# Performance work log

Hardware: AMD Instinct MI355X
Metric: run time of the kernel (lower is better)

Reference implementation:

```python
import jax, jax.numpy as jnp
import numpy as np

N = 100000
E = 1600000
DIN = 128
H = 4
C1 = 32   # hidden_dim per head, layer 1
C2 = 64   # output_dim, layer 2 (heads=1)
NEG_SLOPE = 0.2


def setup_inputs() -> dict:
    key = jax.random.key(0)
    ks = jax.random.split(key, 16)
    x = jax.random.normal(ks[0], (N, DIN), dtype=jnp.float32)
    src = jax.random.randint(ks[1], (E,), 0, N, dtype=jnp.int64)
    off = jax.random.randint(ks[2], (E,), 1, N, dtype=jnp.int64)
    dst = (src + off) % N  # guaranteed no self loops
    edge_index = jnp.stack([src, dst], axis=0)
    edge_weight = jax.random.uniform(ks[3], (E,), dtype=jnp.float32)
    g = 0.1
    # layer 1 params (heads=4, concat)
    W1 = jax.random.normal(ks[4], (DIN, H * C1), dtype=jnp.float32) * g
    att_src1 = jax.random.normal(ks[5], (H, C1), dtype=jnp.float32) * g
    att_dst1 = jax.random.normal(ks[6], (H, C1), dtype=jnp.float32) * g
    att_edge1 = jax.random.normal(ks[7], (H, C1), dtype=jnp.float32) * g
    We1 = jax.random.normal(ks[8], (1, H * C1), dtype=jnp.float32) * g
    b1 = jnp.zeros((H * C1,), dtype=jnp.float32)
    # layer 2 params (heads=1, no concat)
    W2 = jax.random.normal(ks[9], (H * C1, C2), dtype=jnp.float32) * g
    att_src2 = jax.random.normal(ks[10], (1, C2), dtype=jnp.float32) * g
    att_dst2 = jax.random.normal(ks[11], (1, C2), dtype=jnp.float32) * g
    att_edge2 = jax.random.normal(ks[12], (1, C2), dtype=jnp.float32) * g
    We2 = jax.random.normal(ks[13], (1, C2), dtype=jnp.float32) * g
    b2 = jnp.zeros((C2,), dtype=jnp.float32)
    return dict(x=x, edge_index=edge_index, edge_weight=edge_weight,
                W1=W1, att_src1=att_src1, att_dst1=att_dst1, att_edge1=att_edge1, We1=We1, b1=b1,
                W2=W2, att_src2=att_src2, att_dst2=att_dst2, att_edge2=att_edge2, We2=We2, b2=b2)


def gat_conv(x, src, dst, ew, W, a_src, a_dst, a_edge, We, b, heads, out_ch, concat):
    n = x.shape[0]
    xs = (x @ W).reshape(n, heads, out_ch)                 # [N,H,C]
    alpha_src = (xs * a_src[None]).sum(-1)                 # [N,H]
    alpha_dst = (xs * a_dst[None]).sum(-1)                 # [N,H]
    e = (ew[:, None] @ We).reshape(-1, heads, out_ch)      # [E,H,C]
    alpha_edge = (e * a_edge[None]).sum(-1)                # [E,H]
    alpha = alpha_src[src] + alpha_dst[dst] + alpha_edge   # [E,H]
    alpha = jax.nn.leaky_relu(alpha, NEG_SLOPE)
    # segment softmax over destination nodes (every node has a self loop)
    m = jax.ops.segment_max(alpha, dst, num_segments=n)
    ex = jnp.exp(alpha - m[dst])
    s = jax.ops.segment_sum(ex, dst, num_segments=n)
    att = ex / (s[dst] + 1e-16)                            # [E,H]
    out = jax.ops.segment_sum(xs[src] * att[:, :, None], dst, num_segments=n)  # [N,H,C]
    out = out.reshape(n, heads * out_ch) if concat else out.mean(axis=1)
    return out + b


def reference(x, edge_index, edge_weight,
              W1, att_src1, att_dst1, att_edge1, We1, b1,
              W2, att_src2, att_dst2, att_edge2, We2, b2):
    n = x.shape[0]
    src, dst = edge_index[0], edge_index[1]
    # add self loops with fill_value='mean' for edge weights (PyG default)
    si = jnp.arange(n, dtype=src.dtype)
    src2 = jnp.concatenate([src, si])
    dst2 = jnp.concatenate([dst, si])
    ew2 = jnp.concatenate([edge_weight, jnp.full((n,), edge_weight.mean(), dtype=edge_weight.dtype)])
    h = gat_conv(x, src2, dst2, ew2, W1, att_src1, att_dst1, att_edge1, We1, b1, H, C1, True)
    h = jax.nn.elu(h)
    # dropout is identity in eval mode
    out = gat_conv(h, src2, dst2, ew2, W2, att_src2, att_dst2, att_edge2, We2, b2, 1, C2, False)
    return out
```

## Files before the change

### kernel.cpp

```cpp
#include <hip/hip_runtime.h>
#include <math.h>

#define NN 100000
#define NE 1600000
#define DIN 128
#define NH 4
#define C1 32
#define C2 64
#define NEG 0.2f

#define SCAN_CHUNK 1024
#define NBLK ((NN + SCAN_CHUNK - 1) / SCAN_CHUNK)

#define NBUCK 8
#define BUCKN (NN / NBUCK)
#define CAPB 300000
#define BIN_CHUNK 4096
#define NBINBLK ((NE + BIN_CHUNK - 1) / BIN_CHUNK)

__device__ __forceinline__ unsigned bf16rtn(float f) {
    unsigned b = __float_as_uint(f);
    return (b + 0x7FFFu + ((b >> 16) & 1u)) >> 16;
}
__device__ __forceinline__ unsigned pack2bf(float lo, float hi) {
    return bf16rtn(lo) | (bf16rtn(hi) << 16);
}

__global__ void k_setup(const float* __restrict__ We1, const float* __restrict__ ae1,
                        const float* __restrict__ We2, const float* __restrict__ ae2,
                        float* __restrict__ params) {
    __shared__ float sm[128];
    int t = threadIdx.x;
    sm[t] = We1[t] * ae1[t];
    __syncthreads();
    if (t < 4) {
        float s = 0.f;
        for (int c = 0; c < 32; c++) s += sm[t * 32 + c];
        params[2 + t] = s;
    }
    __syncthreads();
    if (t < 64) sm[t] = We2[t] * ae2[t];
    __syncthreads();
    if (t == 0) {
        float s = 0.f;
        for (int c = 0; c < 64; c++) s += sm[c];
        params[6] = s;
        params[1] = params[0] / (float)NE;
    }
}

__global__ void k_binA(const int* __restrict__ srcI, const int* __restrict__ dstI,
                       const float* __restrict__ ew, int* __restrict__ bcur,
                       int* __restrict__ bdst, int2* __restrict__ bse,
                       float* __restrict__ params) {
    __shared__ int hcnt[NBUCK], hbase[NBUCK], hoff[NBUCK];
    int t = threadIdx.x;
    int e0 = blockIdx.x * BIN_CHUNK;
    if (t < NBUCK) hcnt[t] = 0;
    __syncthreads();
    for (int i = t; i < BIN_CHUNK; i += 256) {
        int e = e0 + i;
        if (e < NE) atomicAdd(&hcnt[dstI[e] / BUCKN], 1);
    }
    __syncthreads();
    if (t < NBUCK) { hbase[t] = atomicAdd(&bcur[t], hcnt[t]); hoff[t] = 0; }
    __syncthreads();
    float locw = 0.f;
    for (int i = t; i < BIN_CHUNK; i += 256) {
        int e = e0 + i;
        if (e < NE) {
            int d = dstI[e];
            float w = ew[e];
            locw += w;
            int b = d / BUCKN;
            int p = b * CAPB + hbase[b] + atomicAdd(&hoff[b], 1);
            bdst[p] = d;
            bse[p] = make_int2(srcI[e], __float_as_int(w));
        }
    }
    for (int o = 32; o > 0; o >>= 1) locw += __shfl_down(locw, o, 64);
    if ((t & 63) == 0) atomicAdd(&params[0], locw);
}

__global__ void k_histB(const int* __restrict__ bdst, const int* __restrict__ bcur,
                        int* __restrict__ deg) {
    int b = blockIdx.x & (NBUCK - 1);
    int slice = blockIdx.x >> 3;
    int cnt = bcur[b];
    int lo = b * CAPB;
    int per = (cnt + 255) / 256;
    int s0 = lo + slice * per;
    int s1 = min(s0 + per, lo + cnt);
    for (int i = s0 + threadIdx.x; i < s1; i += 256)
        atomicAdd(&deg[bdst[i]], 1);
}

__global__ void k_scanA(const int* __restrict__ deg, int* __restrict__ bsum) {
    __shared__ int ws[4];
    int b = blockIdx.x;
    int base = b * SCAN_CHUNK;
    int t = threadIdx.x;
    int s = 0;
    for (int i = t; i < SCAN_CHUNK; i += 256) {
        int idx = base + i;
        if (idx < NN) s += deg[idx];
    }
    for (int o = 32; o > 0; o >>= 1) s += __shfl_down(s, o, 64);
    int lane = t & 63, wid = t >> 6;
    if (lane == 0) ws[wid] = s;
    __syncthreads();
    if (t == 0) bsum[b] = ws[0] + ws[1] + ws[2] + ws[3];
}

__global__ void k_scanB(const int* __restrict__ bsum, int* __restrict__ bpre,
                        int* __restrict__ rowptr) {
    __shared__ int wtot[2];
    int t = threadIdx.x;
    int lane = t & 63, wid = t >> 6;
    int v = (t < NBLK) ? bsum[t] : 0;
    int inc = v;
    for (int o = 1; o < 64; o <<= 1) { int u = __shfl_up(inc, o, 64); if (lane >= o) inc += u; }
    if (lane == 63) wtot[wid] = inc;
    __syncthreads();
    if (wid == 1) inc += wtot[0];
    if (t < NBLK) bpre[t] = inc - v;
    if (t == NBLK - 1) rowptr[NN] = inc;
}

__global__ void k_scanC(const int* __restrict__ deg, const int* __restrict__ bpre,
                        int* __restrict__ rowptr, int* __restrict__ cursor) {
    __shared__ int wtot[4];
    int b = blockIdx.x;
    int t = threadIdx.x;
    int lane = t & 63, wid = t >> 6;
    int idx0 = b * SCAN_CHUNK + t * 4;
    int d[4];
    int s = 0;
    #pragma unroll
    for (int j = 0; j < 4; j++) {
        int idx = idx0 + j;
        d[j] = (idx < NN) ? deg[idx] : 0;
        s += d[j];
    }
    int inc = s;
    for (int o = 1; o < 64; o <<= 1) { int u = __shfl_up(inc, o, 64); if (lane >= o) inc += u; }
    if (lane == 63) wtot[wid] = inc;
    __syncthreads();
    int add = bpre[b];
    for (int w = 0; w < wid; w++) add += wtot[w];
    int excl = inc - s + add;
    #pragma unroll
    for (int j = 0; j < 4; j++) {
        int idx = idx0 + j;
        if (idx < NN) { rowptr[idx] = excl; cursor[idx] = excl; }
        excl += d[j];
    }
}

__global__ void k_binB(const int* __restrict__ bdst, const int2* __restrict__ bse,
                       const int* __restrict__ bcur, int* __restrict__ cursor,
                       int2* __restrict__ edge2) {
    int b = blockIdx.x & (NBUCK - 1);
    int slice = blockIdx.x >> 3;
    int cnt = bcur[b];
    int lo = b * CAPB;
    int per = (cnt + 255) / 256;
    int s0 = lo + slice * per;
    int s1 = min(s0 + per, lo + cnt);
    for (int i = s0 + threadIdx.x; i < s1; i += 256) {
        int d = bdst[i];
        int idx = atomicAdd(&cursor[d], 1);
        edge2[idx] = bse[i];
    }
}


__global__ void __launch_bounds__(256, 6)
k_gemm1(const float* __restrict__ x, const float* __restrict__ W1,
        const float* __restrict__ asv, const float* __restrict__ adv,
        unsigned* __restrict__ xs1b, float* __restrict__ as1, float* __restrict__ ad1) {
    __shared__ unsigned xt[64 * 65];
    int t = threadIdx.x;
    int r0 = blockIdx.x * 64;
    for (int i = t; i < 2048; i += 256) {
        int row = i >> 5;
        int c4 = i & 31;
        float4 v = (r0 + row < NN) ? ((const float4*)x)[(size_t)(r0 + row) * 32 + c4]
                                   : make_float4(0.f, 0.f, 0.f, 0.f);
        xt[row * 65 + c4 * 2]     = pack2bf(v.x, v.y);
        xt[row * 65 + c4 * 2 + 1] = pack2bf(v.z, v.w);
    }
    __syncthreads();
    int wid = t >> 6, lane = t & 63;
    int row = r0 + lane;
    int c0 = __builtin_amdgcn_readfirstlane(wid * 32);
    float acc[32];
    #pragma unroll
    for (int c = 0; c < 32; c++) acc[c] = 0.f;
    const unsigned* xr = &xt[lane * 65];
    const float* wp = W1 + c0;
    #pragma unroll 4
    for (int k2 = 0; k2 < 64; k2++) {
        unsigned v = xr[k2];
        float x0 = __uint_as_float(v << 16);
        float x1 = __uint_as_float(v & 0xFFFF0000u);
        const float* w0 = wp + (2 * k2) * 128;
        const float* w1 = w0 + 128;
        #pragma unroll
        for (int c = 0; c < 32; c++) acc[c] += x0 * w0[c] + x1 * w1[c];
    }
    if (row < NN) {
        unsigned* orow = xs1b + (size_t)row * 64 + wid * 16;
        #pragma unroll
        for (int j = 0; j < 4; j++) {
            uint4 pk;
            pk.x = pack2bf(acc[8*j+0], acc[8*j+1]);
            pk.y = pack2bf(acc[8*j+2], acc[8*j+3]);
            pk.z = pack2bf(acc[8*j+4], acc[8*j+5]);
            pk.w = pack2bf(acc[8*j+6], acc[8*j+7]);
            *(uint4*)(orow + 4*j) = pk;
        }
        float ps = 0.f, pd = 0.f;
        #pragma unroll
        for (int c = 0; c < 32; c++) { ps += acc[c] * asv[c0 + c]; pd += acc[c] * adv[c0 + c]; }
        as1[row * 4 + wid] = ps;
        ad1[row * 4 + wid] = pd;
    }
}


__global__ void k_agg1(const unsigned* __restrict__ xs1b, const float* __restrict__ as1,
                       const float* __restrict__ ad1, const int* __restrict__ rowptr,
                       const int2* __restrict__ edge2,
                       const float* __restrict__ params, const float* __restrict__ b1,
                       unsigned* __restrict__ h1b) {
    int wid = threadIdx.x >> 6, lane = threadIdx.x & 63;
    int n = blockIdx.x * 4 + wid;
    if (n >= NN) return;
    int h4 = lane & 3;
    int h  = lane >> 4;
    float ceP  = params[2 + h4];
    float adnP = ad1[n * 4 + h4];
    float meanw = params[1];
    float aself = as1[n * 4 + h] + ad1[n * 4 + h] + meanw * params[2 + h];
    aself = aself > 0.f ? aself : NEG * aself;
    float qs = __expf(aself);
    unsigned us = xs1b[(size_t)n * 64 + lane];
    float s  = qs;
    float ax = qs * __uint_as_float(us << 16);
    float ay = qs * __uint_as_float(us & 0xFFFF0000u);
    int lo = rowptr[n], hi = rowptr[n + 1];
    for (int base = lo; base < hi; base += 16) {
        int e = lane >> 2;
        int idx = base + e;
        int cx = 0;
        float q = 0.f;
        if (idx < hi) {
            int2 cv = edge2[idx];
            cx = cv.x;
            float a = as1[cx * 4 + h4] + adnP + __int_as_float(cv.y) * ceP;
            a = a > 0.f ? a : NEG * a;
            q = __expf(a);
        }
        int m = hi - base; if (m > 16) m = 16;
        int j = 0;
        for (; j + 8 <= m; j += 8) {
            int cj[8]; float qj[8]; unsigned vv[8];
            #pragma unroll
            for (int u = 0; u < 8; u++) {
                cj[u] = __shfl(cx, 4 * (j + u), 64);
                qj[u] = __shfl(q, 4 * (j + u) + h, 64);
            }
            #pragma unroll
            for (int u = 0; u < 8; u++) vv[u] = xs1b[(size_t)cj[u] * 64 + lane];
            #pragma unroll
            for (int u = 0; u < 8; u++) {
                s += qj[u];
                ax += qj[u] * __uint_as_float(vv[u] << 16);
                ay += qj[u] * __uint_as_float(vv[u] & 0xFFFF0000u);
            }
        }
        for (; j < m; j++) {
            int cj = __shfl(cx, 4 * j, 64);
            float qj = __shfl(q, 4 * j + h, 64);
            unsigned u = xs1b[(size_t)cj * 64 + lane];
            s += qj;
            ax += qj * __uint_as_float(u << 16);
            ay += qj * __uint_as_float(u & 0xFFFF0000u);
        }
    }
    float inv = 1.0f / (s + 1e-16f);
    float o0 = ax * inv + b1[2 * lane];
    float o1 = ay * inv + b1[2 * lane + 1];
    o0 = o0 > 0.f ? o0 : (__expf(o0) - 1.0f);
    o1 = o1 > 0.f ? o1 : (__expf(o1) - 1.0f);
    h1b[(size_t)n * 64 + lane] = pack2bf(o0, o1);
}


__global__ void __launch_bounds__(256, 6)
k_gemm2(const unsigned* __restrict__ h1b, const float* __restrict__ W2,
        const float* __restrict__ asv, const float* __restrict__ adv,
        unsigned* __restrict__ xs2b, float* __restrict__ as2, float* __restrict__ ad2) {
    __shared__ unsigned xt[64 * 65];
    __shared__ float pp[2][4][64];
    int t = threadIdx.x;
    int r0 = blockIdx.x * 64;
    for (int i = t; i < 1024; i += 256) {
        int row = i >> 4;
        int q = i & 15;
        uint4 v = (r0 + row < NN) ? ((const uint4*)h1b)[(size_t)(r0 + row) * 16 + q]
                                  : make_uint4(0u, 0u, 0u, 0u);
        unsigned* dst = &xt[row * 65 + q * 4];
        dst[0] = v.x; dst[1] = v.y; dst[2] = v.z; dst[3] = v.w;
    }
    __syncthreads();
    int wid = t >> 6, lane = t & 63;
    int row = r0 + lane;
    int c0 = __builtin_amdgcn_readfirstlane(wid * 16);
    float acc[16];
    #pragma unroll
    for (int c = 0; c < 16; c++) acc[c] = 0.f;
    const unsigned* xr = &xt[lane * 65];
    const float* wp = W2 + c0;
    #pragma unroll 4
    for (int k2 = 0; k2 < 64; k2++) {
        unsigned v = xr[k2];
        float x0 = __uint_as_float(v << 16);
        float x1 = __uint_as_float(v & 0xFFFF0000u);
        const float* w0 = wp + (2 * k2) * 64;
        const float* w1 = w0 + 64;
        #pragma unroll
        for (int c = 0; c < 16; c++) acc[c] += x0 * w0[c] + x1 * w1[c];
    }
    float ps = 0.f, pd = 0.f;
    #pragma unroll
    for (int c = 0; c < 16; c++) { ps += acc[c] * asv[c0 + c]; pd += acc[c] * adv[c0 + c]; }
    pp[0][wid][lane] = ps;
    pp[1][wid][lane] = pd;
    if (row < NN) {
        unsigned* orow = xs2b + (size_t)row * 32 + wid * 8;
        #pragma unroll
        for (int j = 0; j < 2; j++) {
            uint4 pk;
            pk.x = pack2bf(acc[8*j+0], acc[8*j+1]);
            pk.y = pack2bf(acc[8*j+2], acc[8*j+3]);
            pk.z = pack2bf(acc[8*j+4], acc[8*j+5]);
            pk.w = pack2bf(acc[8*j+6], acc[8*j+7]);
            *(uint4*)(orow + 4*j) = pk;
        }
    }
    __syncthreads();
    if (wid == 0 && row < NN) {
        as2[row] = pp[0][0][lane] + pp[0][1][lane] + pp[0][2][lane] + pp[0][3][lane];
        ad2[row] = pp[1][0][lane] + pp[1][1][lane] + pp[1][2][lane] + pp[1][3][lane];
    }
}


__global__ void k_agg2(const unsigned short* __restrict__ xs2h, const float* __restrict__ as2,
                       const float* __restrict__ ad2, const int* __restrict__ rowptr,
                       const int2* __restrict__ edge2,
                       const float* __restrict__ params, const float* __restrict__ b2,
                       float* __restrict__ out) {
    int wid = threadIdx.x >> 6, lane = threadIdx.x & 63;
    int n = blockIdx.x * 4 + wid;
    if (n >= NN) return;
    float ce = params[6];
    float meanw = params[1];
    float adn = ad2[n];
    float aself = as2[n] + adn + meanw * ce;
    aself = aself > 0.f ? aself : NEG * aself;
    float qs = __expf(aself);
    float s = qs;
    float ac = qs * __uint_as_float(((unsigned)xs2h[(size_t)n * 64 + lane]) << 16);
    int lo = rowptr[n], hi = rowptr[n + 1];
    for (int base = lo; base < hi; base += 64) {
        int idx = base + lane;
        int cx = 0;
        float q = 0.f;
        if (idx < hi) {
            int2 cv = edge2[idx];
            cx = cv.x;
            float a = as2[cx] + adn + __int_as_float(cv.y) * ce;
            a = a > 0.f ? a : NEG * a;
            q = __expf(a);
        }
        int m = hi - base; if (m > 64) m = 64;
        int j = 0;
        for (; j + 8 <= m; j += 8) {
            int cj[8]; float qj[8]; unsigned short vv[8];
            #pragma unroll
            for (int u = 0; u < 8; u++) {
                cj[u] = __shfl(cx, j + u, 64);
                qj[u] = __shfl(q, j + u, 64);
            }
            #pragma unroll
            for (int u = 0; u < 8; u++) vv[u] = xs2h[(size_t)cj[u] * 64 + lane];
            #pragma unroll
            for (int u = 0; u < 8; u++) {
                s += qj[u];
                ac += qj[u] * __uint_as_float(((unsigned)vv[u]) << 16);
            }
        }
        for (; j < m; j++) {
            int cj = __shfl(cx, j, 64);
            float qj = __shfl(q, j, 64);
            float v = __uint_as_float(((unsigned)xs2h[(size_t)cj * 64 + lane]) << 16);
            s += qj;
            ac += qj * v;
        }
    }
    out[(size_t)n * 64 + lane] = ac / (s + 1e-16f) + b2[lane];
}

extern "C" void kernel_launch(void* const* d_in, const int* in_sizes, int n_in,
                              void* d_out, int out_size, void* d_ws, size_t ws_size,
                              hipStream_t stream) {
    const float* x    = (const float*)d_in[0];
    const int*   ei   = (const int*)d_in[1];
    const float* ew   = (const float*)d_in[2];
    const float* W1   = (const float*)d_in[3];
    const float* as1v = (const float*)d_in[4];
    const float* ad1v = (const float*)d_in[5];
    const float* ae1v = (const float*)d_in[6];
    const float* We1  = (const float*)d_in[7];
    const float* b1   = (const float*)d_in[8];
    const float* W2   = (const float*)d_in[9];
    const float* as2v = (const float*)d_in[10];
    const float* ad2v = (const float*)d_in[11];
    const float* ae2v = (const float*)d_in[12];
    const float* We2  = (const float*)d_in[13];
    const float* b2   = (const float*)d_in[14];
    const int* srcI = ei;
    const int* dstI = ei + NE;

    float* wsf = (float*)d_ws;
    size_t off = 0;
    auto alloc = [&](size_t nelts) { float* p = wsf + off; off += (nelts + 63) & ~(size_t)63; return p; };
    float*    params = alloc(64);
    int*      deg    = (int*)alloc(NN);
    int*      bcur   = (int*)alloc(64);
    int*      rowptr = (int*)alloc(NN + 1);
    int*      cursor = (int*)alloc(NN);
    int*      bsum   = (int*)alloc(NBLK);
    int*      bpre   = (int*)alloc(NBLK);
    size_t    binsOff = off;
    int*      bdst   = (int*)alloc((size_t)NBUCK * CAPB);
    int2*     bse    = (int2*)alloc((size_t)NBUCK * CAPB * 2);
    int2*     edge2  = (int2*)alloc((size_t)NE * 2);
    float*    as1    = alloc(NN * 4);
    float*    ad1    = alloc(NN * 4);
    unsigned* h1b    = (unsigned*)alloc((size_t)NN * 64);
    unsigned* xs1b   = (unsigned*)(wsf + binsOff);
    unsigned* xs2b   = xs1b;
    float*    as2 = as1;
    float*    ad2 = ad1;

    hipMemsetAsync(d_ws, 0, (64 + 100032 + 64) * sizeof(float), stream);

    k_binA <<<NBINBLK, 256, 0, stream>>>(srcI, dstI, ew, bcur, bdst, bse, params);
    k_histB<<<2048, 256, 0, stream>>>(bdst, bcur, deg);
    k_scanA<<<NBLK, 256, 0, stream>>>(deg, bsum);
    k_scanB<<<1, 128, 0, stream>>>(bsum, bpre, rowptr);
    k_scanC<<<NBLK, 256, 0, stream>>>(deg, bpre, rowptr, cursor);
    k_binB <<<2048, 256, 0, stream>>>(bdst, bse, bcur, cursor, edge2);
    k_setup<<<1, 128, 0, stream>>>(We1, ae1v, We2, ae2v, params);
    k_gemm1<<<(NN + 63) / 64, 256, 0, stream>>>(x, W1, as1v, ad1v, xs1b, as1, ad1);
    k_agg1 <<<25000, 256, 0, stream>>>(xs1b, as1, ad1, rowptr, edge2, params, b1, h1b);
    k_gemm2<<<(NN + 63) / 64, 256, 0, stream>>>(h1b, W2, as2v, ad2v, xs2b, as2, ad2);
    k_agg2 <<<25000, 256, 0, stream>>>((const unsigned short*)xs2b, as2, ad2, rowptr, edge2, params, b2, (float*)d_out);
}
```

Before: 429.6 us.

## Use bf16 MFMA for both node GEMMs with pre-packed weight fragments

A new prep kernel packs W1 and W2 into bf16 MFMA B-fragment layout. Both node-feature GEMMs now run on mfma_f32_16x16x32_bf16 instead of scalar FMA loops that read fp32 weights from global memory. Results are staged through shared memory to form the bf16 outputs and the attention dot products. This aims to cut GEMM compute time, at the cost of an extra small launch, larger LDS use and lower occupancy bounds for gemm1.

```diff
diff --git a/kernel.cpp b/kernel.cpp
--- a/kernel.cpp
+++ b/kernel.cpp
@@ -18,6 +18,9 @@
 #define BIN_CHUNK 4096
 #define NBINBLK ((NE + BIN_CHUNK - 1) / BIN_CHUNK)
 
+typedef __attribute__((ext_vector_type(8))) short bf16x8;
+typedef __attribute__((ext_vector_type(4))) float f32x4;
+
 __device__ __forceinline__ unsigned bf16rtn(float f) {
     unsigned b = __float_as_uint(f);
     return (b + 0x7FFFu + ((b >> 16) & 1u)) >> 16;
@@ -46,6 +49,37 @@
         for (int c = 0; c < 64; c++) s += sm[c];
         params[6] = s;
         params[1] = params[0] / (float)NE;
+    }
+}
+
+__global__ void k_wprep(const float* __restrict__ W1, const float* __restrict__ W2,
+                        uint4* __restrict__ wfrag1, uint4* __restrict__ wfrag2) {
+    int t = blockIdx.x * 256 + threadIdx.x;
+    if (t < 2048) {
+        int f = t >> 6, l = t & 63;
+        int n = f & 7, kc = f >> 3;
+        int col = n * 16 + (l & 15);
+        int kb = kc * 32 + (l >> 4) * 8;
+        const float* p = W1 + (size_t)kb * 128 + col;
+        uint4 pk;
+        pk.x = pack2bf(p[0], p[128]);
+        pk.y = pack2bf(p[256], p[384]);
+        pk.z = pack2bf(p[512], p[640]);
+        pk.w = pack2bf(p[768], p[896]);
+        wfrag1[t] = pk;
+    } else if (t < 3072) {
+        int s = t - 2048;
+        int f = s >> 6, l = s & 63;
+        int n = f & 3, kc = f >> 2;
+        int col = n * 16 + (l & 15);
+        int kb = kc * 32 + (l >> 4) * 8;
+        const float* p = W2 + (size_t)kb * 64 + col;
+        uint4 pk;
+        pk.x = pack2bf(p[0], p[64]);
+        pk.y = pack2bf(p[128], p[192]);
+        pk.z = pack2bf(p[256], p[320]);
+        pk.w = pack2bf(p[384], p[448]);
+        wfrag2[s] = pk;
     }
 }
 
@@ -175,56 +209,80 @@
 }
 
 
-__global__ void __launch_bounds__(256, 6)
-k_gemm1(const float* __restrict__ x, const float* __restrict__ W1,
+__global__ void __launch_bounds__(256, 4)
+k_gemm1(const float* __restrict__ x, const uint4* __restrict__ wfrag1,
         const float* __restrict__ asv, const float* __restrict__ adv,
         unsigned* __restrict__ xs1b, float* __restrict__ as1, float* __restrict__ ad1) {
-    __shared__ unsigned xt[64 * 65];
-    int t = threadIdx.x;
-    int r0 = blockIdx.x * 64;
-    for (int i = t; i < 2048; i += 256) {
-        int row = i >> 5;
-        int c4 = i & 31;
-        float4 v = (r0 + row < NN) ? ((const float4*)x)[(size_t)(r0 + row) * 32 + c4]
-                                   : make_float4(0.f, 0.f, 0.f, 0.f);
-        xt[row * 65 + c4 * 2]     = pack2bf(v.x, v.y);
-        xt[row * 65 + c4 * 2 + 1] = pack2bf(v.z, v.w);
-    }
+    __shared__ uint4 smem[2112];
+    int t = threadIdx.x;
+    for (int i = t; i < 2048; i += 256) smem[i] = wfrag1[i];
     __syncthreads();
     int wid = t >> 6, lane = t & 63;
-    int row = r0 + lane;
-    int c0 = __builtin_amdgcn_readfirstlane(wid * 32);
-    float acc[32];
-    #pragma unroll
-    for (int c = 0; c < 32; c++) acc[c] = 0.f;
-    const unsigned* xr = &xt[lane * 65];
-    const float* wp = W1 + c0;
-    #pragma unroll 4
-    for (int k2 = 0; k2 < 64; k2++) {
-        unsigned v = xr[k2];
-        float x0 = __uint_as_float(v << 16);
-        float x1 = __uint_as_float(v & 0xFFFF0000u);
-        const float* w0 = wp + (2 * k2) * 128;
-        const float* w1 = w0 + 128;
-        #pragma unroll
-        for (int c = 0; c < 32; c++) acc[c] += x0 * w0[c] + x1 * w1[c];
-    }
+    int r0 = blockIdx.x * 64 + wid * 16;
+    int rowA = r0 + (lane & 15);
+    int kb = (lane >> 4) * 8;
+    bf16x8 afr[4];
+    if (rowA < NN) {
+        const float* xr = x + (size_t)rowA * 128 + kb;
+        #pragma unroll
+        for (int kc = 0; kc < 4; kc++) {
+            float4 u0 = *(const float4*)(xr + kc * 32);
+            float4 u1 = *(const float4*)(xr + kc * 32 + 4);
+            uint4 p = make_uint4(pack2bf(u0.x, u0.y), pack2bf(u0.z, u0.w),
+                                 pack2bf(u1.x, u1.y), pack2bf(u1.z, u1.w));
+            afr[kc] = *(bf16x8*)&p;
+        }
+    } else {
+        uint4 z = make_uint4(0u, 0u, 0u, 0u);
+        #pragma unroll
+        for (int kc = 0; kc < 4; kc++) afr[kc] = *(bf16x8*)&z;
+    }
+    f32x4 acc[8];
+    #pragma unroll
+    for (int n = 0; n < 8; n++) acc[n] = (f32x4){0.f, 0.f, 0.f, 0.f};
+    #pragma unroll
+    for (int kc = 0; kc < 4; kc++) {
+        #pragma unroll
+        for (int n = 0; n < 8; n++) {
+            uint4 bw = smem[(kc * 8 + n) * 64 + lane];
+            acc[n] = __builtin_amdgcn_mfma_f32_16x16x32_bf16(afr[kc], *(bf16x8*)&bw, acc[n], 0, 0, 0);
+        }
+    }
+    __syncthreads();
+    float* ef = (float*)smem + wid * 2112;
+    #pragma unroll
+    for (int n = 0; n < 8; n++) {
+        #pragma unroll
+        for (int r = 0; r < 4; r++) {
+            int rw = (lane >> 4) * 4 + r;
+            int col = n * 16 + (lane & 15);
+            ef[rw * 132 + (col >> 5) * 33 + (col & 31)] = acc[n][r];
+        }
+    }
+    __syncthreads();
+    int rw = lane >> 2, head = lane & 3;
+    int row = r0 + rw;
     if (row < NN) {
-        unsigned* orow = xs1b + (size_t)row * 64 + wid * 16;
+        const float* rb = ef + rw * 132 + head * 33;
+        const float* av = asv + head * 32;
+        const float* dv = adv + head * 32;
+        unsigned* orow = xs1b + (size_t)row * 64 + head * 16;
+        float ps = 0.f, pd = 0.f;
         #pragma unroll
         for (int j = 0; j < 4; j++) {
-            uint4 pk;
-            pk.x = pack2bf(acc[8*j+0], acc[8*j+1]);
-            pk.y = pack2bf(acc[8*j+2], acc[8*j+3]);
-            pk.z = pack2bf(acc[8*j+4], acc[8*j+5]);
-            pk.w = pack2bf(acc[8*j+6], acc[8*j+7]);
-            *(uint4*)(orow + 4*j) = pk;
-        }
-        float ps = 0.f, pd = 0.f;
-        #pragma unroll
-        for (int c = 0; c < 32; c++) { ps += acc[c] * asv[c0 + c]; pd += acc[c] * adv[c0 + c]; }
-        as1[row * 4 + wid] = ps;
-        ad1[row * 4 + wid] = pd;
+            float v[8];
+            #pragma unroll
+            for (int e = 0; e < 8; e++) {
+                v[e] = rb[8 * j + e];
+                ps += v[e] * av[8 * j + e];
+                pd += v[e] * dv[8 * j + e];
+            }
+            uint4 pk = make_uint4(pack2bf(v[0], v[1]), pack2bf(v[2], v[3]),
+                                  pack2bf(v[4], v[5]), pack2bf(v[6], v[7]));
+            *(uint4*)(orow + 4 * j) = pk;
+        }
+        as1[row * 4 + head] = ps;
+        ad1[row * 4 + head] = pd;
     }
 }
 
@@ -299,62 +357,76 @@
 
 
 __global__ void __launch_bounds__(256, 6)
-k_gemm2(const unsigned* __restrict__ h1b, const float* __restrict__ W2,
+k_gemm2(const unsigned* __restrict__ h1b, const uint4* __restrict__ wfrag2,
         const float* __restrict__ asv, const float* __restrict__ adv,
         unsigned* __restrict__ xs2b, float* __restrict__ as2, float* __restrict__ ad2) {
-    __shared__ unsigned xt[64 * 65];
-    __shared__ float pp[2][4][64];
-    int t = threadIdx.x;
-    int r0 = blockIdx.x * 64;
-    for (int i = t; i < 1024; i += 256) {
-        int row = i >> 4;
-        int q = i & 15;
-        uint4 v = (r0 + row < NN) ? ((const uint4*)h1b)[(size_t)(r0 + row) * 16 + q]
-                                  : make_uint4(0u, 0u, 0u, 0u);
-        unsigned* dst = &xt[row * 65 + q * 4];
-        dst[0] = v.x; dst[1] = v.y; dst[2] = v.z; dst[3] = v.w;
-    }
+    __shared__ uint4 smem[1056];
+    int t = threadIdx.x;
+    for (int i = t; i < 1024; i += 256) smem[i] = wfrag2[i];
     __syncthreads();
     int wid = t >> 6, lane = t & 63;
-    int row = r0 + lane;
-    int c0 = __builtin_amdgcn_readfirstlane(wid * 16);
-    float acc[16];
-    #pragma unroll
-    for (int c = 0; c < 16; c++) acc[c] = 0.f;
-    const unsigned* xr = &xt[lane * 65];
-    const float* wp = W2 + c0;
-    #pragma unroll 4
-    for (int k2 = 0; k2 < 64; k2++) {
-        unsigned v = xr[k2];
-        float x0 = __uint_as_float(v << 16);
-        float x1 = __uint_as_float(v & 0xFFFF0000u);
-        const float* w0 = wp + (2 * k2) * 64;
-        const float* w1 = w0 + 64;
-        #pragma unroll
-        for (int c = 0; c < 16; c++) acc[c] += x0 * w0[c] + x1 * w1[c];
-    }
+    int r0 = blockIdx.x * 64 + wid * 16;
+    int rowA = r0 + (lane & 15);
+    bf16x8 afr[4];
+    if (rowA < NN) {
+        const uint4* hr = (const uint4*)(h1b + (size_t)rowA * 64);
+        #pragma unroll
+        for (int kc = 0; kc < 4; kc++) {
+            uint4 p = hr[kc * 4 + (lane >> 4)];
+            afr[kc] = *(bf16x8*)&p;
+        }
+    } else {
+        uint4 z = make_uint4(0u, 0u, 0u, 0u);
+        #pragma unroll
+        for (int kc = 0; kc < 4; kc++) afr[kc] = *(bf16x8*)&z;
+    }
+    f32x4 acc[4];
+    #pragma unroll
+    for (int n = 0; n < 4; n++) acc[n] = (f32x4){0.f, 0.f, 0.f, 0.f};
+    #pragma unroll
+    for (int kc = 0; kc < 4; kc++) {
+        #pragma unroll
+        for (int n = 0; n < 4; n++) {
+            uint4 bw = smem[(kc * 4 + n) * 64 + lane];
+            acc[n] = __builtin_amdgcn_mfma_f32_16x16x32_bf16(afr[kc], *(bf16x8*)&bw, acc[n], 0, 0, 0);
+        }
+    }
+    __syncthreads();
+    float* ef = (float*)smem + wid * 1056;
+    #pragma unroll
+    for (int n = 0; n < 4; n++) {
+        #pragma unroll
+        for (int r = 0; r < 4; r++) {
+            int rw = (lane >> 4) * 4 + r;
+            int col = n * 16 + (lane & 15);
+            ef[rw * 66 + (col >> 5) * 33 + (col & 31)] = acc[n][r];
+        }
+    }
+    __syncthreads();
+    int rw = lane >> 2, q = lane & 3;
+    int row = r0 + rw;
+    const float* rb = ef + rw * 66 + (q >> 1) * 33 + (q & 1) * 16;
+    const float* av = asv + q * 16;
+    const float* dv = adv + q * 16;
     float ps = 0.f, pd = 0.f;
-    #pragma unroll
-    for (int c = 0; c < 16; c++) { ps += acc[c] * asv[c0 + c]; pd += acc[c] * adv[c0 + c]; }
-    pp[0][wid][lane] = ps;
-    pp[1][wid][lane] = pd;
-    if (row < NN) {
-        unsigned* orow = xs2b + (size_t)row * 32 + wid * 8;
-        #pragma unroll
-        for (int j = 0; j < 2; j++) {
-            uint4 pk;
-            pk.x = pack2bf(acc[8*j+0], acc[8*j+1]);
-            pk.y = pack2bf(acc[8*j+2], acc[8*j+3]);
-            pk.z = pack2bf(acc[8*j+4], acc[8*j+5]);
-            pk.w = pack2bf(acc[8*j+6], acc[8*j+7]);
-            *(uint4*)(orow + 4*j) = pk;
-        }
-    }
-    __syncthreads();
-    if (wid == 0 && row < NN) {
-        as2[row] = pp[0][0][lane] + pp[0][1][lane] + pp[0][2][lane] + pp[0][3][lane];
-        ad2[row] = pp[1][0][lane] + pp[1][1][lane] + pp[1][2][lane] + pp[1][3][lane];
-    }
+    unsigned pk[4];
+    #pragma unroll
+    for (int j = 0; j < 2; j++) {
+        float v[8];
+        #pragma unroll
+        for (int e = 0; e < 8; e++) {
+            v[e] = rb[8 * j + e];
+            ps += v[e] * av[8 * j + e];
+            pd += v[e] * dv[8 * j + e];
+        }
+        pk[0] = pack2bf(v[0], v[1]); pk[1] = pack2bf(v[2], v[3]);
+        pk[2] = pack2bf(v[4], v[5]); pk[3] = pack2bf(v[6], v[7]);
+        if (row < NN)
+            *(uint4*)(xs2b + (size_t)row * 32 + q * 8 + 4 * j) = make_uint4(pk[0], pk[1], pk[2], pk[3]);
+    }
+    ps += __shfl_xor(ps, 1, 64); ps += __shfl_xor(ps, 2, 64);
+    pd += __shfl_xor(pd, 1, 64); pd += __shfl_xor(pd, 2, 64);
+    if (q == 0 && row < NN) { as2[row] = ps; ad2[row] = pd; }
 }
 
 
@@ -445,6 +517,8 @@
     int*      cursor = (int*)alloc(NN);
     int*      bsum   = (int*)alloc(NBLK);
     int*      bpre   = (int*)alloc(NBLK);
+    uint4*    wfrag1 = (uint4*)alloc(8192);
+    uint4*    wfrag2 = (uint4*)alloc(4096);
     size_t    binsOff = off;
     int*      bdst   = (int*)alloc((size_t)NBUCK * CAPB);
     int2*     bse    = (int2*)alloc((size_t)NBUCK * CAPB * 2);
@@ -459,6 +533,7 @@
 
     hipMemsetAsync(d_ws, 0, (64 + 100032 + 64) * sizeof(float), stream);
 
+    k_wprep<<<12, 256, 0, stream>>>(W1, W2, wfrag1, wfrag2);
     k_binA <<<NBINBLK, 256, 0, stream>>>(srcI, dstI, ew, bcur, bdst, bse, params);
     k_histB<<<2048, 256, 0, stream>>>(bdst, bcur, deg);
     k_scanA<<<NBLK, 256, 0, stream>>>(deg, bsum);
@@ -466,8 +541,8 @@
     k_scanC<<<NBLK, 256, 0, stream>>>(deg, bpre, rowptr, cursor);
     k_binB <<<2048, 256, 0, stream>>>(bdst, bse, bcur, cursor, edge2);
     k_setup<<<1, 128, 0, stream>>>(We1, ae1v, We2, ae2v, params);
-    k_gemm1<<<(NN + 63) / 64, 256, 0, stream>>>(x, W1, as1v, ad1v, xs1b, as1, ad1);
+    k_gemm1<<<(NN + 63) / 64, 256, 0, stream>>>(x, wfrag1, as1v, ad1v, xs1b, as1, ad1);
     k_agg1 <<<25000, 256, 0, stream>>>(xs1b, as1, ad1, rowptr, edge2, params, b1, h1b);
-    k_gemm2<<<(NN + 63) / 64, 256, 0, stream>>>(h1b, W2, as2v, ad2v, xs2b, as2, ad2);
+    k_gemm2<<<(NN + 63) / 64, 256, 0, stream>>>(h1b, wfrag2, as2v, ad2v, xs2b, as2, ad2);
     k_agg2 <<<25000, 256, 0, stream>>>((const unsigned short*)xs2b, as2, ad2, rowptr, edge2, params, b2, (float*)d_out);
 }
```

After: 368.0 us. 14.3% less time.
